# Kernel optimization log

Hardware: AMD Instinct MI355X
Metric: run time of the kernel (lower is better)

Reference implementation:

```python
import jax, jax.numpy as jnp
import numpy as np

N = 100000      # nodes
E = 1600000     # edges (before self-loops)
IN = 128        # in_dim
HID = 128       # hidden_dim
H = 4           # heads
D = HID // H    # head_dim = 32
L = 3           # n_layers
G = 128         # graphs in batch
NEG_SLOPE = 0.2 # PyG GATConv default leaky_relu slope
BN_EPS = 1e-5


def setup_inputs() -> dict:
    key = jax.random.key(0)
    ks = jax.random.split(key, 16)
    x = jax.random.normal(ks[0], (N, IN), dtype=jnp.float32)
    edge_index = jax.random.randint(ks[1], (2, E), 0, N, dtype=jnp.int64)
    batch = jnp.sort(jax.random.randint(ks[2], (N,), 0, G, dtype=jnp.int64))
    # stacked per-layer GATConv params (in_dim == hidden_dim so all layers stack)
    W = jax.random.normal(ks[3], (L, HID, HID), dtype=jnp.float32) * (1.0 / np.sqrt(HID))
    att_src = jax.random.normal(ks[4], (L, H, D), dtype=jnp.float32) * 0.1
    att_dst = jax.random.normal(ks[5], (L, H, D), dtype=jnp.float32) * 0.1
    bias = jax.random.normal(ks[6], (L, HID), dtype=jnp.float32) * 0.01
    # BatchNorm1d (eval mode: running stats)
    gamma = 1.0 + 0.1 * jax.random.normal(ks[7], (L, HID), dtype=jnp.float32)
    beta = 0.01 * jax.random.normal(ks[8], (L, HID), dtype=jnp.float32)
    bn_mean = jnp.zeros((L, HID), dtype=jnp.float32)
    bn_var = jnp.ones((L, HID), dtype=jnp.float32)
    # MLP head: Linear(HID, HID//2) -> ReLU -> Linear(HID//2, 1)
    Wh1 = jax.random.normal(ks[9], (HID, HID // 2), dtype=jnp.float32) * (1.0 / np.sqrt(HID))
    bh1 = jnp.zeros((HID // 2,), dtype=jnp.float32)
    Wh2 = jax.random.normal(ks[10], (HID // 2, 1), dtype=jnp.float32) * (1.0 / np.sqrt(HID // 2))
    bh2 = jnp.zeros((1,), dtype=jnp.float32)
    return {"x": x, "edge_index": edge_index, "batch": batch, "W": W,
            "att_src": att_src, "att_dst": att_dst, "bias": bias,
            "gamma": gamma, "beta": beta, "bn_mean": bn_mean, "bn_var": bn_var,
            "Wh1": Wh1, "bh1": bh1, "Wh2": Wh2, "bh2": bh2}


def _gat_conv(x, src, dst, W_l, asrc, adst, b):
    # x: [N, F_in]; src/dst: [E+N] (self-loops included); returns [N, H*D]
    h = (x @ W_l).reshape(N, H, D)                      # [N,H,D]
    a_s = jnp.einsum('nhd,hd->nh', h, asrc)             # [N,H]
    a_d = jnp.einsum('nhd,hd->nh', h, adst)
    e = jax.nn.leaky_relu(a_s[src] + a_d[dst], NEG_SLOPE)  # [Etot,H]
    # segment softmax over incoming edges per destination node
    e_max = jax.ops.segment_max(e, dst, num_segments=N)    # [N,H]
    p = jnp.exp(e - e_max[dst])
    denom = jax.ops.segment_sum(p, dst, num_segments=N)    # [N,H]
    alpha = p / (denom[dst] + 1e-16)                        # [Etot,H]
    msg = h[src] * alpha[:, :, None]                        # [Etot,H,D]
    out = jax.ops.segment_sum(msg, dst, num_segments=N)     # [N,H,D]
    return out.reshape(N, H * D) + b


def reference(x, edge_index, batch, W, att_src, att_dst, bias,
              gamma, beta, bn_mean, bn_var, Wh1, bh1, Wh2, bh2):
    # add self-loops once (PyG GATConv default add_self_loops=True)
    loop = jnp.arange(N, dtype=edge_index.dtype)
    src = jnp.concatenate([edge_index[0], loop])
    dst = jnp.concatenate([edge_index[1], loop])
    for l in range(L):
        x = _gat_conv(x, src, dst, W[l], att_src[l], att_dst[l], bias[l])
        x = jnp.maximum(x, 0.0)
        # BatchNorm1d, eval mode (dropout is identity in eval)
        x = (x - bn_mean[l]) * (gamma[l] / jnp.sqrt(bn_var[l] + BN_EPS)) + beta[l]
    # global mean pool over graphs
    sums = jax.ops.segment_sum(x, batch, num_segments=G)            # [G,HID]
    cnts = jax.ops.segment_sum(jnp.ones((N,), x.dtype), batch, num_segments=G)
    pooled = sums / jnp.maximum(cnts, 1.0)[:, None]
    hdn = jnp.maximum(pooled @ Wh1 + bh1, 0.0)
    return (hdn @ Wh2 + bh2).squeeze(-1)                            # [G]
```

## Files before the change

### kernel.cpp

```cpp
#include <hip/hip_runtime.h>
#include <hip/hip_fp16.h>


typedef __bf16 bf16x8 __attribute__((ext_vector_type(8)));
typedef float  f32x4  __attribute__((ext_vector_type(4)));
typedef unsigned int u32x4 __attribute__((ext_vector_type(4)));

#define WLSZ 36864
#define MAXBKT 800
#define BCAP   4096

__device__ __forceinline__ int foff(int l, int d, int n, int k) {
    int ct = n >> 4, li = n & 15;
    int ks = k >> 5, bq = (k >> 3) & 3, j = k & 7;
    return l * WLSZ + (((ks * 18) + d * 9 + ct) * 64 + (bq << 4) + li) * 8 + j;
}

__global__ __launch_bounds__(256)
void k_front(const int* __restrict__ ei, unsigned int* __restrict__ bkt,
             int* __restrict__ bcnt, float* __restrict__ gsum,
             int* __restrict__ gcnt, const int* __restrict__ batch,
             const float* __restrict__ gamma, const float* __restrict__ beta,
             const float* __restrict__ mean, const float* __restrict__ var,
             float* __restrict__ bn_mul, float* __restrict__ bn_add,
             const float* __restrict__ W, const float* __restrict__ asrc,
             const float* __restrict__ adst, __bf16* __restrict__ WF,
             int Ne, int Nn, int nbkt, int Gg, int nBB) {
    __shared__ int lcnt[MAXBKT];
    __shared__ int lbase[MAXBKT];
    int bb = blockIdx.x;
    int tid = threadIdx.x;

    if (bb < nBB) {
        int gid = bb * 256 + tid;
        if (gid < Gg * 128) gsum[gid] = 0.f;
        for (int i = tid; i < nbkt; i += 256) lcnt[i] = 0;
        __syncthreads();
        int chunk0 = bb * 2048;
        int nnz = Ne + Nn;
        for (int i = 0; i < 8; ++i) {
            int e = chunk0 + i * 256 + tid;
            if (e < nnz) {
                int d = (e < Ne) ? ei[Ne + e] : (e - Ne);
                atomicAdd(&lcnt[d >> 7], 1);
            }
        }
        __syncthreads();
        for (int b = tid; b < nbkt; b += 256) {
            int c = lcnt[b];
            lbase[b] = (c > 0) ? atomicAdd(&bcnt[b], c) : 0;
            lcnt[b] = 0;
        }
        __syncthreads();
        for (int i = 0; i < 8; ++i) {
            int e = chunk0 + i * 256 + tid;
            if (e < nnz) {
                int s, d;
                if (e < Ne) { s = ei[e]; d = ei[Ne + e]; }
                else        { s = e - Ne; d = e - Ne; }
                int b = d >> 7;
                int r = atomicAdd(&lcnt[b], 1);
                bkt[(long)b * BCAP + lbase[b] + r] = ((unsigned)s << 7) | (unsigned)(d & 127);
            }
        }
    } else if (bb < nBB + 192) {
        int gid = (bb - nBB) * 256 + tid;
        if (gid < 384) {
            float sc = gamma[gid] / sqrtf(var[gid] + 1e-5f);
            bn_mul[gid] = sc;
            bn_add[gid] = beta[gid] - mean[gid] * sc;
        }
        if (gid < 3 * 128 * 128) {
            int l = gid >> 14;
            int k = (gid >> 7) & 127;
            int n = gid & 127;
            float f = W[gid];
            __bf16 h = (__bf16)f;
            WF[foff(l, 0, n, k)] = h;
            WF[foff(l, 1, n, k)] = (__bf16)(f - (float)h);
        }
        if (gid < 3 * 128 * 8) {
            int l = gid >> 10;
            int r = gid & 1023;
            int k = r >> 3;
            int j = r & 7;
            int hh = j & 3;
            const float* av = (j < 4 ? asrc : adst) + l * 128 + hh * 32;
            const float* wp = W + l * 16384 + k * 128 + hh * 32;
            float sum = 0.f;
#pragma unroll
            for (int d = 0; d < 32; ++d) sum = fmaf(wp[d], av[d], sum);
            __bf16 h = (__bf16)sum;
            WF[foff(l, 0, 128 + j, k)] = h;
            WF[foff(l, 1, 128 + j, k)] = (__bf16)(sum - (float)h);
        }
        if (gid < 3 * 128 * 8) {
            int l = gid >> 10;
            int r = gid & 1023;
            int k = r >> 3;
            int j = r & 7;
            WF[foff(l, 0, 136 + j, k)] = (__bf16)0.f;
            WF[foff(l, 1, 136 + j, k)] = (__bf16)0.f;
        }
    } else {
        int g = tid;
        if (g < Gg) {
            int lo = 0, hi = Nn;
            while (lo < hi) { int mid = (lo + hi) >> 1; if (batch[mid] < g) lo = mid + 1; else hi = mid; }
            int lo2 = lo, hi2 = Nn;
            while (lo2 < hi2) { int mid = (lo2 + hi2) >> 1; if (batch[mid] < g + 1) lo2 = mid + 1; else hi2 = mid; }
            gcnt[g] = lo2 - lo;
        }
    }
}

__global__ __launch_bounds__(256)
void k_bscatter2(const unsigned int* __restrict__ bkt, const int* __restrict__ bcnt,
                 int* __restrict__ rowstart, int* __restrict__ rowdeg,
                 int* __restrict__ colv, int Nn) {
    __shared__ int h[128], sc0[128], sc1[128];
    int b = blockIdx.x;
    int tid = threadIdx.x;
    if (tid < 128) h[tid] = 0;
    __syncthreads();
    int cnt = bcnt[b];
    const unsigned int* bp = bkt + (long)b * BCAP;
    for (int i = tid; i < cnt; i += 256) atomicAdd(&h[bp[i] & 127], 1);
    __syncthreads();
    int cntN = (tid < 128) ? h[tid] : 0;
    if (tid < 128) sc0[tid] = cntN;
    __syncthreads();
    int* src = sc0; int* dst = sc1;
    for (int off = 1; off < 128; off <<= 1) {
        if (tid < 128) {
            int x = src[tid];
            if (tid >= off) x += src[tid - off];
            dst[tid] = x;
        }
        __syncthreads();
        int* tw = src; src = dst; dst = tw;
    }
    int node = b * 128 + tid;
    if (tid < 128) {
        int st = b * BCAP + (src[tid] - cntN);
        h[tid] = st;
        if (node < Nn) { rowstart[node] = st; rowdeg[node] = cntN; }
    }
    __syncthreads();
    for (int i = tid; i < cnt; i += 256) {
        unsigned int e = bp[i];
        int pos = atomicAdd(&h[e & 127], 1);
        colv[pos] = (int)(e >> 7);
    }
}

__global__ __launch_bounds__(256, 4)
void k_gemm_mfma(const float* __restrict__ X, const __bf16* __restrict__ WF,
                 __half* __restrict__ Hout,
                 float* __restrict__ as_, float* __restrict__ ad_, int Nn) {
    int t = threadIdx.x;
    int w = t >> 6;
    int lane = t & 63;
    int li = lane & 15;
    int b  = lane >> 4;
    long row = (long)blockIdx.x * 64 + w * 16 + li;
    long rA = (row > Nn - 1) ? (Nn - 1) : row;

    f32x4 acc[9];
#pragma unroll
    for (int ct = 0; ct < 9; ++ct) acc[ct] = (f32x4){0.f, 0.f, 0.f, 0.f};

#pragma unroll
    for (int ks = 0; ks < 4; ++ks) {
        int k0 = ks * 32 + 8 * b;
        const float* xp = X + rA * 128 + k0;
        float4 f0 = *(const float4*)xp;
        float4 f1 = *(const float4*)(xp + 4);
        float af[8] = {f0.x, f0.y, f0.z, f0.w, f1.x, f1.y, f1.z, f1.w};
        bf16x8 ahi, alo;
#pragma unroll
        for (int j = 0; j < 8; ++j) {
            __bf16 h = (__bf16)af[j];
            ahi[j] = h;
            alo[j] = (__bf16)(af[j] - (float)h);
        }
        const __bf16* wk = WF + (ks * 18) * 512 + lane * 8;
#pragma unroll
        for (int ct = 0; ct < 9; ++ct) {
            bf16x8 bhi = *(const bf16x8*)(wk + ct * 512);
            bf16x8 blo = *(const bf16x8*)(wk + (9 + ct) * 512);
            acc[ct] = __builtin_amdgcn_mfma_f32_16x16x32_bf16(bhi, ahi, acc[ct], 0, 0, 0);
            acc[ct] = __builtin_amdgcn_mfma_f32_16x16x32_bf16(bhi, alo, acc[ct], 0, 0, 0);
            acc[ct] = __builtin_amdgcn_mfma_f32_16x16x32_bf16(blo, ahi, acc[ct], 0, 0, 0);
        }
    }

    if (row < Nn) {
        __half* op = Hout + row * 128 + 4 * b;
#pragma unroll
        for (int ct = 0; ct < 8; ++ct) {
            union { __half2 h2[2]; uint2 u; } pk;
            pk.h2[0] = __floats2half2_rn(acc[ct][0], acc[ct][1]);
            pk.h2[1] = __floats2half2_rn(acc[ct][2], acc[ct][3]);
            *(uint2*)(op + ct * 16) = pk.u;
        }
        if (b == 0)
            *(float4*)(as_ + 4 * row) = make_float4(acc[8][0], acc[8][1],
                                                    acc[8][2], acc[8][3]);
        else if (b == 1)
            *(float4*)(ad_ + 4 * row) = make_float4(acc[8][0], acc[8][1],
                                                    acc[8][2], acc[8][3]);
    }
}

#define LEAKY(x) ((x) > 0.f ? (x) : 0.2f * (x))

template <bool POOL>
__global__ __launch_bounds__(256)
void k_aggregate(const __half* __restrict__ Hb, const float* __restrict__ as_,
                 const float* __restrict__ ad_, const int* __restrict__ rowstart,
                 const int* __restrict__ rowdeg,
                 const int* __restrict__ col, const float* __restrict__ bias,
                 const float* __restrict__ bn_mul, const float* __restrict__ bn_add,
                 float* __restrict__ Xout, const int* __restrict__ batch,
                 float* __restrict__ gsum, int Nn) {
    __shared__ int2 s_pk[4][64][4];
    __shared__ float s_out[POOL ? 4 : 1][POOL ? 128 : 1];
    __shared__ int s_g[POOL ? 4 : 1];
    int w = threadIdx.x >> 6;
    int n = (blockIdx.x << 2) + w;
    int lane = threadIdx.x & 63;
    bool active = (n < Nn);
    if (!POOL && !active) return;
    if (POOL && lane == 0) s_g[w] = active ? batch[n] : -1;

    if (active) {
        int start = rowstart[n];
        int deg = rowdeg[n];

        if (deg <= 64) {
            int hh = lane & 3;
            int slot = lane >> 2;
            float adn = ad_[4 * n + hh];
            float esc[4]; int scl[4];
#pragma unroll
            for (int c = 0; c < 4; ++c) {
                int eidx = (c << 4) + slot;
                float e = -1e30f; int s = 0;
                if (eidx < deg) {
                    s = col[start + eidx];
                    e = LEAKY(as_[4 * s + hh] + adn);
                }
                esc[c] = e; scl[c] = s;
            }
            float m = fmaxf(fmaxf(esc[0], esc[1]), fmaxf(esc[2], esc[3]));
#pragma unroll
            for (int msk = 4; msk < 64; msk <<= 1) m = fmaxf(m, __shfl_xor(m, msk, 64));
            float p[4];
            float den = 0.f;
#pragma unroll
            for (int c = 0; c < 4; ++c) { p[c] = __expf(esc[c] - m); den += p[c]; }
#pragma unroll
            for (int msk = 4; msk < 64; msk <<= 1) den += __shfl_xor(den, msk, 64);
            float inv = 1.f / (den + 1e-16f);
#pragma unroll
            for (int c = 0; c < 4; ++c) {
                int2 pk;
                pk.x = scl[c] << 8;
                pk.y = __float_as_int(p[c] * inv);
                s_pk[w][(c << 4) + slot][hh] = pk;
            }

            int quarter = lane >> 4;
            int li = lane & 15;
            int hB = li >> 2;
            int cByte = li << 4;
            const char* hb8 = (const char*)Hb;
            float acc[8];
#pragma unroll
            for (int i = 0; i < 8; ++i) acc[i] = 0.f;

            int nit = (deg + 7) >> 3;
            int2 pk0 = s_pk[w][quarter][hB];
            int2 pk1 = s_pk[w][quarter + 4][hB];
            float a0 = __int_as_float(pk0.y);
            float a1 = __int_as_float(pk1.y);
            u32x4 r0 = *(const u32x4*)(hb8 + pk0.x + cByte);
            u32x4 r1 = *(const u32x4*)(hb8 + pk1.x + cByte);
            for (int it = 1; it < nit; ++it) {
                int e0 = (it << 3) + quarter;
                int2 q0 = s_pk[w][e0][hB];
                int2 q1 = s_pk[w][e0 + 4][hB];
                u32x4 t0 = *(const u32x4*)(hb8 + q0.x + cByte);
                u32x4 t1 = *(const u32x4*)(hb8 + q1.x + cByte);
                const __half* h0 = (const __half*)&r0;
                const __half* h1 = (const __half*)&r1;
#pragma unroll
                for (int q = 0; q < 8; ++q) {
                    acc[q] = fmaf(__half2float(h0[q]), a0, acc[q]);
                    acc[q] = fmaf(__half2float(h1[q]), a1, acc[q]);
                }
                r0 = t0; r1 = t1;
                a0 = __int_as_float(q0.y);
                a1 = __int_as_float(q1.y);
            }
            {
                const __half* h0 = (const __half*)&r0;
                const __half* h1 = (const __half*)&r1;
#pragma unroll
                for (int q = 0; q < 8; ++q) {
                    acc[q] = fmaf(__half2float(h0[q]), a0, acc[q]);
                    acc[q] = fmaf(__half2float(h1[q]), a1, acc[q]);
                }
            }
#pragma unroll
            for (int i = 0; i < 8; ++i) {
                float v = acc[i];
                v += __shfl_xor(v, 16, 64);
                v += __shfl_xor(v, 32, 64);
                acc[i] = v;
            }
            if (lane < 16) {
                int c0 = li << 3;
                float4 bz0 = *(const float4*)(bias + c0);
                float4 bz1 = *(const float4*)(bias + c0 + 4);
                float4 m0 = *(const float4*)(bn_mul + c0);
                float4 m1 = *(const float4*)(bn_mul + c0 + 4);
                float4 a0v = *(const float4*)(bn_add + c0);
                float4 a1v = *(const float4*)(bn_add + c0 + 4);
                float4 o0, o1;
                o0.x = fmaf(fmaxf(acc[0] + bz0.x, 0.f), m0.x, a0v.x);
                o0.y = fmaf(fmaxf(acc[1] + bz0.y, 0.f), m0.y, a0v.y);
                o0.z = fmaf(fmaxf(acc[2] + bz0.z, 0.f), m0.z, a0v.z);
                o0.w = fmaf(fmaxf(acc[3] + bz0.w, 0.f), m0.w, a0v.w);
                o1.x = fmaf(fmaxf(acc[4] + bz1.x, 0.f), m1.x, a1v.x);
                o1.y = fmaf(fmaxf(acc[5] + bz1.y, 0.f), m1.y, a1v.y);
                o1.z = fmaf(fmaxf(acc[6] + bz1.z, 0.f), m1.z, a1v.z);
                o1.w = fmaf(fmaxf(acc[7] + bz1.w, 0.f), m1.w, a1v.w);
                if (!POOL) {
                    *(float4*)(Xout + (long)n * 128 + c0)     = o0;
                    *(float4*)(Xout + (long)n * 128 + c0 + 4) = o1;
                } else {
                    *(float4*)(&s_out[w][c0])     = o0;
                    *(float4*)(&s_out[w][c0 + 4]) = o1;
                }
            }
        } else {
            int end = start + deg;
            int hh = lane & 3;
            float adn = ad_[n * 4 + hh];
            float m = -1e30f;
            for (int base = start; base < end; base += 16) {
                int idx = base + (lane >> 2);
                float sc = -1e30f;
                if (idx < end) {
                    int s = col[idx];
                    float e = as_[s * 4 + hh] + adn;
                    sc = LEAKY(e);
                }
                m = fmaxf(m, sc);
            }
            for (int msk = 4; msk < 64; msk <<= 1) m = fmaxf(m, __shfl_xor(m, msk, 64));
            float den = 0.f;
            for (int base = start; base < end; base += 16) {
                int idx = base + (lane >> 2);
                if (idx < end) {
                    int s = col[idx];
                    float e = as_[s * 4 + hh] + adn;
                    e = LEAKY(e);
                    den += __expf(e - m);
                }
            }
            for (int msk = 4; msk < 64; msk <<= 1) den += __shfl_xor(den, msk, 64);
            int hB = lane >> 4;
            float mB   = __shfl(m, hB, 64);
            float invB = 1.f / (__shfl(den, hB, 64) + 1e-16f);
            float adB  = ad_[n * 4 + hB];
            int c0 = lane << 1;
            float acc0 = 0.f, acc1 = 0.f;
            for (int i = start; i < end; ++i) {
                int s = col[i];
                float e = as_[s * 4 + hB] + adB;
                e = LEAKY(e);
                float alpha = __expf(e - mB) * invB;
                float2 hv = __half22float2(*(const __half2*)(Hb + (long)s * 128 + c0));
                acc0 = fmaf(hv.x, alpha, acc0);
                acc1 = fmaf(hv.y, alpha, acc1);
            }
            float v0 = acc0 + bias[c0], v1 = acc1 + bias[c0 + 1];
            v0 = fmaxf(v0, 0.f); v1 = fmaxf(v1, 0.f);
            v0 = fmaf(v0, bn_mul[c0], bn_add[c0]);
            v1 = fmaf(v1, bn_mul[c0 + 1], bn_add[c0 + 1]);
            if (!POOL) {
                *(float2*)(Xout + (long)n * 128 + c0) = make_float2(v0, v1);
            } else {
                s_out[w][c0]     = v0;
                s_out[w][c0 + 1] = v1;
            }
        }
    } else if (POOL) {
        if (lane < 16) {
            int c0 = (lane & 15) << 3;
#pragma unroll
            for (int i = 0; i < 8; ++i) s_out[w][c0 + i] = 0.f;
        }
    }

    if (POOL) {
        __syncthreads();
        int tid = threadIdx.x;
        if (tid < 128) {
            int g0 = s_g[0], g1 = s_g[1], g2 = s_g[2], g3 = s_g[3];
            float v0 = s_out[0][tid], v1 = s_out[1][tid];
            float v2 = s_out[2][tid], v3 = s_out[3][tid];
            if (g0 == g1 && g1 == g2 && g2 == g3) {
                if (g0 >= 0) atomicAdd(&gsum[g0 * 128 + tid], v0 + v1 + v2 + v3);
            } else {
                if (g0 >= 0) atomicAdd(&gsum[g0 * 128 + tid], v0);
                if (g1 >= 0) atomicAdd(&gsum[g1 * 128 + tid], v1);
                if (g2 >= 0) atomicAdd(&gsum[g2 * 128 + tid], v2);
                if (g3 >= 0) atomicAdd(&gsum[g3 * 128 + tid], v3);
            }
        }
    }
}

__global__ __launch_bounds__(64)
void k_head(const float* __restrict__ gsum, const int* __restrict__ gcnt,
            const float* __restrict__ Wh1, const float* __restrict__ bh1,
            const float* __restrict__ Wh2, const float* __restrict__ bh2,
            float* __restrict__ outp) {
    __shared__ float pooled[128];
    int g = blockIdx.x;
    int j = threadIdx.x;
    int cnt = gcnt[g];
    float inv = 1.f / (float)(cnt > 1 ? cnt : 1);
    pooled[j]      = gsum[g * 128 + j] * inv;
    pooled[j + 64] = gsum[g * 128 + 64 + j] * inv;
    __syncthreads();
    float acc = bh1[j];
    for (int k = 0; k < 128; ++k) acc = fmaf(pooled[k], Wh1[k * 64 + j], acc);
    acc = fmaxf(acc, 0.f);
    float prod = acc * Wh2[j];
    for (int msk = 1; msk < 64; msk <<= 1) prod += __shfl_xor(prod, msk, 64);
    if (j == 0) outp[g] = prod + bh2[0];
}

extern "C" void kernel_launch(void* const* d_in, const int* in_sizes, int n_in,
                              void* d_out, int out_size, void* d_ws, size_t ws_size,
                              hipStream_t stream) {
    const float* x       = (const float*)d_in[0];
    const int*   ei      = (const int*)d_in[1];
    const int*   batch   = (const int*)d_in[2];
    const float* W       = (const float*)d_in[3];
    const float* att_src = (const float*)d_in[4];
    const float* att_dst = (const float*)d_in[5];
    const float* bias    = (const float*)d_in[6];
    const float* gamma   = (const float*)d_in[7];
    const float* beta    = (const float*)d_in[8];
    const float* bn_mean = (const float*)d_in[9];
    const float* bn_var  = (const float*)d_in[10];
    const float* Wh1     = (const float*)d_in[11];
    const float* bh1     = (const float*)d_in[12];
    const float* Wh2     = (const float*)d_in[13];
    const float* bh2     = (const float*)d_in[14];
    float* out = (float*)d_out;

    const int Nn = in_sizes[0] / 128;
    const int Ne = in_sizes[1] / 2;
    const int Gg = out_size;
    const int nnz = Ne + Nn;
    const int nbkt = (Nn + 127) / 128;
    const int nBB = (nnz + 2047) / 2048;

    char* ws = (char*)d_ws;
    size_t off = 0;
    auto alloc = [&](size_t bytes) -> char* {
        char* p = ws + off;
        off = (off + bytes + 255) & ~(size_t)255;
        return p;
    };
    float*        bufA     = (float*)alloc((size_t)Nn * 128 * 4);
    __half*       bufH     = (__half*)alloc((size_t)Nn * 128 * 2);
    float*        as_      = (float*)alloc((size_t)Nn * 4 * 4);
    float*        ad_      = (float*)alloc((size_t)Nn * 4 * 4);
    int*          rowstart = (int*)alloc((size_t)Nn * 4);
    int*          rowdeg   = (int*)alloc((size_t)Nn * 4);
    int*          col      = (int*)alloc((size_t)nbkt * BCAP * 4);
    float*        bn_mul   = (float*)alloc(384 * 4);
    float*        bn_add   = (float*)alloc(384 * 4);
    float*        gsum     = (float*)alloc((size_t)Gg * 128 * 4);
    int*          gcnt     = (int*)alloc((size_t)Gg * 4);
    __bf16*       WtF      = (__bf16*)alloc((size_t)3 * WLSZ * 2);
    unsigned int* bkt      = (unsigned int*)alloc((size_t)nbkt * BCAP * 4);
    int*          bcnt     = (int*)alloc((size_t)nbkt * 4);

    hipMemsetAsync(bcnt, 0, (size_t)nbkt * 4, stream);
    k_front<<<nBB + 193, 256, 0, stream>>>(ei, bkt, bcnt, gsum, gcnt, batch,
                                           gamma, beta, bn_mean, bn_var,
                                           bn_mul, bn_add, W, att_src, att_dst,
                                           WtF, Ne, Nn, nbkt, Gg, nBB);
    k_bscatter2<<<nbkt, 256, 0, stream>>>(bkt, bcnt, rowstart, rowdeg, col, Nn);

    const float* cur = x;
    for (int l = 0; l < 3; ++l) {
        k_gemm_mfma<<<(Nn + 63) / 64, 256, 0, stream>>>(cur, WtF + l * WLSZ,
                                                        bufH, as_, ad_, Nn);
        if (l < 2)
            k_aggregate<false><<<(Nn + 3) / 4, 256, 0, stream>>>(
                bufH, as_, ad_, rowstart, rowdeg, col, bias + l * 128,
                bn_mul + l * 128, bn_add + l * 128, bufA, batch, gsum, Nn);
        else
            k_aggregate<true><<<(Nn + 3) / 4, 256, 0, stream>>>(
                bufH, as_, ad_, rowstart, rowdeg, col, bias + l * 128,
                bn_mul + l * 128, bn_add + l * 128, bufA, batch, gsum, Nn);
        cur = bufA;
    }

    k_head<<<Gg, 64, 0, stream>>>(gsum, gcnt, Wh1, bh1, Wh2, bh2, out);
}
```

Baseline: 504.2 us.

## Process two nodes per wavefront in GAT aggregation when both degrees are small

Restructures the aggregation kernel so each 64-lane wavefront handles two destination nodes, one per 32-lane half, whenever both have degree at most 32, which is the common case with an average degree near 17. The goal is to cut the idle lanes and per-node overhead of the earlier one-node-per-wave scheme, where most softmax slots and gather lanes did nothing. Pairs that include a higher-degree node fall back to processing the two nodes one after another with the old full-wave and big-degree paths. The cost is more shuffle and branch logic, scalar rather than vectorised output stores, and a slowdown when either node in a pair exceeds 32 edges.

Measured after the change: 506.7 us. No clear change (+0.5%).

```diff
diff --git a/kernel.cpp b/kernel.cpp
--- a/kernel.cpp
+++ b/kernel.cpp
@@ -215,6 +215,153 @@
 
 #define LEAKY(x) ((x) > 0.f ? (x) : 0.2f * (x))
 
+__device__ __forceinline__ void agg_full(
+    const __half* __restrict__ Hb, const float* __restrict__ as_,
+    const float* __restrict__ ad_, const int* __restrict__ col,
+    const float* __restrict__ bias, const float* __restrict__ bn_mul,
+    const float* __restrict__ bn_add, int2 (*spk)[4],
+    int n, int start, int deg, int lane, float* orow) {
+    int hh = lane & 3;
+    int slot = lane >> 2;
+    float adn = ad_[4 * n + hh];
+    float esc[4]; int scl[4];
+#pragma unroll
+    for (int c = 0; c < 4; ++c) {
+        int eidx = (c << 4) + slot;
+        float e = -1e30f; int s = 0;
+        if (eidx < deg) {
+            s = col[start + eidx];
+            e = LEAKY(as_[4 * s + hh] + adn);
+        }
+        esc[c] = e; scl[c] = s;
+    }
+    float m = fmaxf(fmaxf(esc[0], esc[1]), fmaxf(esc[2], esc[3]));
+#pragma unroll
+    for (int msk = 4; msk < 64; msk <<= 1) m = fmaxf(m, __shfl_xor(m, msk, 64));
+    float p[4];
+    float den = 0.f;
+#pragma unroll
+    for (int c = 0; c < 4; ++c) { p[c] = __expf(esc[c] - m); den += p[c]; }
+#pragma unroll
+    for (int msk = 4; msk < 64; msk <<= 1) den += __shfl_xor(den, msk, 64);
+    float inv = 1.f / (den + 1e-16f);
+#pragma unroll
+    for (int c = 0; c < 4; ++c) {
+        int2 pk;
+        pk.x = scl[c] << 8;
+        pk.y = __float_as_int(p[c] * inv);
+        spk[(c << 4) + slot][hh] = pk;
+    }
+
+    int quarter = lane >> 4;
+    int li = lane & 15;
+    int hB = li >> 2;
+    int cByte = li << 4;
+    const char* hb8 = (const char*)Hb;
+    float acc[8];
+#pragma unroll
+    for (int i = 0; i < 8; ++i) acc[i] = 0.f;
+
+    int nit = (deg + 7) >> 3;
+    int2 pk0 = spk[quarter][hB];
+    int2 pk1 = spk[quarter + 4][hB];
+    float a0 = __int_as_float(pk0.y);
+    float a1 = __int_as_float(pk1.y);
+    u32x4 r0 = *(const u32x4*)(hb8 + pk0.x + cByte);
+    u32x4 r1 = *(const u32x4*)(hb8 + pk1.x + cByte);
+    for (int it = 1; it < nit; ++it) {
+        int e0 = (it << 3) + quarter;
+        int2 q0 = spk[e0][hB];
+        int2 q1 = spk[e0 + 4][hB];
+        u32x4 t0 = *(const u32x4*)(hb8 + q0.x + cByte);
+        u32x4 t1 = *(const u32x4*)(hb8 + q1.x + cByte);
+        const __half* h0 = (const __half*)&r0;
+        const __half* h1 = (const __half*)&r1;
+#pragma unroll
+        for (int q = 0; q < 8; ++q) {
+            acc[q] = fmaf(__half2float(h0[q]), a0, acc[q]);
+            acc[q] = fmaf(__half2float(h1[q]), a1, acc[q]);
+        }
+        r0 = t0; r1 = t1;
+        a0 = __int_as_float(q0.y);
+        a1 = __int_as_float(q1.y);
+    }
+    {
+        const __half* h0 = (const __half*)&r0;
+        const __half* h1 = (const __half*)&r1;
+#pragma unroll
+        for (int q = 0; q < 8; ++q) {
+            acc[q] = fmaf(__half2float(h0[q]), a0, acc[q]);
+            acc[q] = fmaf(__half2float(h1[q]), a1, acc[q]);
+        }
+    }
+#pragma unroll
+    for (int i = 0; i < 8; ++i) {
+        float v = acc[i];
+        v += __shfl_xor(v, 16, 64);
+        v += __shfl_xor(v, 32, 64);
+        acc[i] = v;
+    }
+    if (lane < 16) {
+        int c0 = li << 3;
+#pragma unroll
+        for (int i = 0; i < 8; ++i) {
+            float v = fmaxf(acc[i] + bias[c0 + i], 0.f);
+            orow[c0 + i] = fmaf(v, bn_mul[c0 + i], bn_add[c0 + i]);
+        }
+    }
+}
+
+__device__ __forceinline__ void agg_big(
+    const __half* __restrict__ Hb, const float* __restrict__ as_,
+    const float* __restrict__ ad_, const int* __restrict__ col,
+    const float* __restrict__ bias, const float* __restrict__ bn_mul,
+    const float* __restrict__ bn_add,
+    int n, int start, int deg, int lane, float* orow) {
+    int end = start + deg;
+    int hh = lane & 3;
+    float adn = ad_[n * 4 + hh];
+    float m = -1e30f;
+    for (int base = start; base < end; base += 16) {
+        int idx = base + (lane >> 2);
+        float sc = -1e30f;
+        if (idx < end) {
+            int s = col[idx];
+            sc = LEAKY(as_[s * 4 + hh] + adn);
+        }
+        m = fmaxf(m, sc);
+    }
+    for (int msk = 4; msk < 64; msk <<= 1) m = fmaxf(m, __shfl_xor(m, msk, 64));
+    float den = 0.f;
+    for (int base = start; base < end; base += 16) {
+        int idx = base + (lane >> 2);
+        if (idx < end) {
+            int s = col[idx];
+            float e = LEAKY(as_[s * 4 + hh] + adn);
+            den += __expf(e - m);
+        }
+    }
+    for (int msk = 4; msk < 64; msk <<= 1) den += __shfl_xor(den, msk, 64);
+    int hB = lane >> 4;
+    float mB   = __shfl(m, hB, 64);
+    float invB = 1.f / (__shfl(den, hB, 64) + 1e-16f);
+    float adB  = ad_[n * 4 + hB];
+    int c0 = lane << 1;
+    float acc0 = 0.f, acc1 = 0.f;
+    for (int i = start; i < end; ++i) {
+        int s = col[i];
+        float e = LEAKY(as_[s * 4 + hB] + adB);
+        float alpha = __expf(e - mB) * invB;
+        float2 hv = __half22float2(*(const __half2*)(Hb + (long)s * 128 + c0));
+        acc0 = fmaf(hv.x, alpha, acc0);
+        acc1 = fmaf(hv.y, alpha, acc1);
+    }
+    float v0 = fmaxf(acc0 + bias[c0], 0.f);
+    float v1 = fmaxf(acc1 + bias[c0 + 1], 0.f);
+    orow[c0]     = fmaf(v0, bn_mul[c0], bn_add[c0]);
+    orow[c0 + 1] = fmaf(v1, bn_mul[c0 + 1], bn_add[c0 + 1]);
+}
+
 template <bool POOL>
 __global__ __launch_bounds__(256)
 void k_aggregate(const __half* __restrict__ Hb, const float* __restrict__ as_,
@@ -225,184 +372,136 @@
                  float* __restrict__ Xout, const int* __restrict__ batch,
                  float* __restrict__ gsum, int Nn) {
     __shared__ int2 s_pk[4][64][4];
-    __shared__ float s_out[POOL ? 4 : 1][POOL ? 128 : 1];
-    __shared__ int s_g[POOL ? 4 : 1];
+    __shared__ float s_out[POOL ? 8 : 1][POOL ? 128 : 1];
+    __shared__ int s_g[POOL ? 8 : 1];
     int w = threadIdx.x >> 6;
-    int n = (blockIdx.x << 2) + w;
     int lane = threadIdx.x & 63;
-    bool active = (n < Nn);
-    if (!POOL && !active) return;
-    if (POOL && lane == 0) s_g[w] = active ? batch[n] : -1;
-
-    if (active) {
-        int start = rowstart[n];
-        int deg = rowdeg[n];
-
-        if (deg <= 64) {
-            int hh = lane & 3;
-            int slot = lane >> 2;
-            float adn = ad_[4 * n + hh];
-            float esc[4]; int scl[4];
-#pragma unroll
-            for (int c = 0; c < 4; ++c) {
-                int eidx = (c << 4) + slot;
-                float e = -1e30f; int s = 0;
-                if (eidx < deg) {
-                    s = col[start + eidx];
-                    e = LEAKY(as_[4 * s + hh] + adn);
+    int half = lane >> 5;
+    int hl = lane & 31;
+    int nbase = (blockIdx.x << 3) + (w << 1);
+    int n = nbase + half;
+    bool active = n < Nn;
+    if (!POOL && nbase >= Nn) return;
+    if (POOL && hl == 0) s_g[(w << 1) + half] = active ? batch[n] : -1;
+
+    int start = active ? rowstart[n] : 0;
+    int deg   = active ? rowdeg[n]   : 0;
+    int degO  = __shfl_xor(deg, 32, 64);
+    int degmax = deg > degO ? deg : degO;
+
+    if (degmax <= 32) {
+        int hh = hl & 3;
+        int slot = hl >> 2;
+        float adn = active ? ad_[4 * n + hh] : 0.f;
+        float esc[4]; int scl[4];
+#pragma unroll
+        for (int c = 0; c < 4; ++c) {
+            int eidx = (c << 3) + slot;
+            float e = -1e30f; int s = 0;
+            if (eidx < deg) {
+                s = col[start + eidx];
+                e = LEAKY(as_[4 * s + hh] + adn);
+            }
+            esc[c] = e; scl[c] = s;
+        }
+        float m = fmaxf(fmaxf(esc[0], esc[1]), fmaxf(esc[2], esc[3]));
+#pragma unroll
+        for (int msk = 4; msk < 32; msk <<= 1) m = fmaxf(m, __shfl_xor(m, msk, 64));
+        float p[4];
+        float den = 0.f;
+#pragma unroll
+        for (int c = 0; c < 4; ++c) { p[c] = __expf(esc[c] - m); den += p[c]; }
+#pragma unroll
+        for (int msk = 4; msk < 32; msk <<= 1) den += __shfl_xor(den, msk, 64);
+        float inv = 1.f / (den + 1e-16f);
+        int hbase = half << 5;
+#pragma unroll
+        for (int c = 0; c < 4; ++c) {
+            int2 pk;
+            pk.x = scl[c] << 8;
+            pk.y = __float_as_int(p[c] * inv);
+            s_pk[w][hbase + (c << 3) + slot][hh] = pk;
+        }
+
+        int q = (hl >> 4) & 1;
+        int li = hl & 15;
+        int hB = li >> 2;
+        int cByte = li << 4;
+        const char* hb8 = (const char*)Hb;
+        float acc[8];
+#pragma unroll
+        for (int i = 0; i < 8; ++i) acc[i] = 0.f;
+
+        int nit = (degmax + 3) >> 2;
+        int2 pk0 = s_pk[w][hbase + q][hB];
+        int2 pk1 = s_pk[w][hbase + q + 2][hB];
+        float a0 = __int_as_float(pk0.y);
+        float a1 = __int_as_float(pk1.y);
+        u32x4 r0 = *(const u32x4*)(hb8 + pk0.x + cByte);
+        u32x4 r1 = *(const u32x4*)(hb8 + pk1.x + cByte);
+        for (int it = 1; it < nit; ++it) {
+            int e0 = (it << 2) + q;
+            int2 q0 = s_pk[w][hbase + e0][hB];
+            int2 q1 = s_pk[w][hbase + e0 + 2][hB];
+            u32x4 t0 = *(const u32x4*)(hb8 + q0.x + cByte);
+            u32x4 t1 = *(const u32x4*)(hb8 + q1.x + cByte);
+            const __half* h0 = (const __half*)&r0;
+            const __half* h1 = (const __half*)&r1;
+#pragma unroll
+            for (int qq = 0; qq < 8; ++qq) {
+                acc[qq] = fmaf(__half2float(h0[qq]), a0, acc[qq]);
+                acc[qq] = fmaf(__half2float(h1[qq]), a1, acc[qq]);
+            }
+            r0 = t0; r1 = t1;
+            a0 = __int_as_float(q0.y);
+            a1 = __int_as_float(q1.y);
+        }
+        {
+            const __half* h0 = (const __half*)&r0;
+            const __half* h1 = (const __half*)&r1;
+#pragma unroll
+            for (int qq = 0; qq < 8; ++qq) {
+                acc[qq] = fmaf(__half2float(h0[qq]), a0, acc[qq]);
+                acc[qq] = fmaf(__half2float(h1[qq]), a1, acc[qq]);
+            }
+        }
+#pragma unroll
+        for (int i = 0; i < 8; ++i) acc[i] += __shfl_xor(acc[i], 16, 64);
+
+        if (hl < 16) {
+            int c0 = li << 3;
+            if (active) {
+#pragma unroll
+                for (int i = 0; i < 8; ++i) {
+                    float v = fmaxf(acc[i] + bias[c0 + i], 0.f);
+                    v = fmaf(v, bn_mul[c0 + i], bn_add[c0 + i]);
+                    if (!POOL) Xout[(long)n * 128 + c0 + i] = v;
+                    else       s_out[(w << 1) + half][c0 + i] = v;
                 }
-                esc[c] = e; scl[c] = s;
-            }
-            float m = fmaxf(fmaxf(esc[0], esc[1]), fmaxf(esc[2], esc[3]));
-#pragma unroll
-            for (int msk = 4; msk < 64; msk <<= 1) m = fmaxf(m, __shfl_xor(m, msk, 64));
-            float p[4];
-            float den = 0.f;
-#pragma unroll
-            for (int c = 0; c < 4; ++c) { p[c] = __expf(esc[c] - m); den += p[c]; }
-#pragma unroll
-            for (int msk = 4; msk < 64; msk <<= 1) den += __shfl_xor(den, msk, 64);
-            float inv = 1.f / (den + 1e-16f);
-#pragma unroll
-            for (int c = 0; c < 4; ++c) {
-                int2 pk;
-                pk.x = scl[c] << 8;
-                pk.y = __float_as_int(p[c] * inv);
-                s_pk[w][(c << 4) + slot][hh] = pk;
-            }
-
-            int quarter = lane >> 4;
-            int li = lane & 15;
-            int hB = li >> 2;
-            int cByte = li << 4;
-            const char* hb8 = (const char*)Hb;
-            float acc[8];
-#pragma unroll
-            for (int i = 0; i < 8; ++i) acc[i] = 0.f;
-
-            int nit = (deg + 7) >> 3;
-            int2 pk0 = s_pk[w][quarter][hB];
-            int2 pk1 = s_pk[w][quarter + 4][hB];
-            float a0 = __int_as_float(pk0.y);
-            float a1 = __int_as_float(pk1.y);
-            u32x4 r0 = *(const u32x4*)(hb8 + pk0.x + cByte);
-            u32x4 r1 = *(const u32x4*)(hb8 + pk1.x + cByte);
-            for (int it = 1; it < nit; ++it) {
-                int e0 = (it << 3) + quarter;
-                int2 q0 = s_pk[w][e0][hB];
-                int2 q1 = s_pk[w][e0 + 4][hB];
-                u32x4 t0 = *(const u32x4*)(hb8 + q0.x + cByte);
-                u32x4 t1 = *(const u32x4*)(hb8 + q1.x + cByte);
-                const __half* h0 = (const __half*)&r0;
-                const __half* h1 = (const __half*)&r1;
-#pragma unroll
-                for (int q = 0; q < 8; ++q) {
-                    acc[q] = fmaf(__half2float(h0[q]), a0, acc[q]);
-                    acc[q] = fmaf(__half2float(h1[q]), a1, acc[q]);
-                }
-                r0 = t0; r1 = t1;
-                a0 = __int_as_float(q0.y);
-                a1 = __int_as_float(q1.y);
-            }
-            {
-                const __half* h0 = (const __half*)&r0;
-                const __half* h1 = (const __half*)&r1;
-#pragma unroll
-                for (int q = 0; q < 8; ++q) {
-                    acc[q] = fmaf(__half2float(h0[q]), a0, acc[q]);
-                    acc[q] = fmaf(__half2float(h1[q]), a1, acc[q]);
-                }
-            }
-#pragma unroll
-            for (int i = 0; i < 8; ++i) {
-                float v = acc[i];
-                v += __shfl_xor(v, 16, 64);
-                v += __shfl_xor(v, 32, 64);
-                acc[i] = v;
-            }
-            if (lane < 16) {
-                int c0 = li << 3;
-                float4 bz0 = *(const float4*)(bias + c0);
-                float4 bz1 = *(const float4*)(bias + c0 + 4);
-                float4 m0 = *(const float4*)(bn_mul + c0);
-                float4 m1 = *(const float4*)(bn_mul + c0 + 4);
-                float4 a0v = *(const float4*)(bn_add + c0);
-                float4 a1v = *(const float4*)(bn_add + c0 + 4);
-                float4 o0, o1;
-                o0.x = fmaf(fmaxf(acc[0] + bz0.x, 0.f), m0.x, a0v.x);
-                o0.y = fmaf(fmaxf(acc[1] + bz0.y, 0.f), m0.y, a0v.y);
-                o0.z = fmaf(fmaxf(acc[2] + bz0.z, 0.f), m0.z, a0v.z);
-                o0.w = fmaf(fmaxf(acc[3] + bz0.w, 0.f), m0.w, a0v.w);
-                o1.x = fmaf(fmaxf(acc[4] + bz1.x, 0.f), m1.x, a1v.x);
-                o1.y = fmaf(fmaxf(acc[5] + bz1.y, 0.f), m1.y, a1v.y);
-                o1.z = fmaf(fmaxf(acc[6] + bz1.z, 0.f), m1.z, a1v.z);
-                o1.w = fmaf(fmaxf(acc[7] + bz1.w, 0.f), m1.w, a1v.w);
-                if (!POOL) {
-                    *(float4*)(Xout + (long)n * 128 + c0)     = o0;
-                    *(float4*)(Xout + (long)n * 128 + c0 + 4) = o1;
-                } else {
-                    *(float4*)(&s_out[w][c0])     = o0;
-                    *(float4*)(&s_out[w][c0 + 4]) = o1;
-                }
-            }
-        } else {
-            int end = start + deg;
-            int hh = lane & 3;
-            float adn = ad_[n * 4 + hh];
-            float m = -1e30f;
-            for (int base = start; base < end; base += 16) {
-                int idx = base + (lane >> 2);
-                float sc = -1e30f;
-                if (idx < end) {
-                    int s = col[idx];
-                    float e = as_[s * 4 + hh] + adn;
-                    sc = LEAKY(e);
-                }
-                m = fmaxf(m, sc);
-            }
-            for (int msk = 4; msk < 64; msk <<= 1) m = fmaxf(m, __shfl_xor(m, msk, 64));
-            float den = 0.f;
-            for (int base = start; base < end; base += 16) {
-                int idx = base + (lane >> 2);
-                if (idx < end) {
-                    int s = col[idx];
-                    float e = as_[s * 4 + hh] + adn;
-                    e = LEAKY(e);
-                    den += __expf(e - m);
-                }
-            }
-            for (int msk = 4; msk < 64; msk <<= 1) den += __shfl_xor(den, msk, 64);
-            int hB = lane >> 4;
-            float mB   = __shfl(m, hB, 64);
-            float invB = 1.f / (__shfl(den, hB, 64) + 1e-16f);
-            float adB  = ad_[n * 4 + hB];
-            int c0 = lane << 1;
-            float acc0 = 0.f, acc1 = 0.f;
-            for (int i = start; i < end; ++i) {
-                int s = col[i];
-                float e = as_[s * 4 + hB] + adB;
-                e = LEAKY(e);
-                float alpha = __expf(e - mB) * invB;
-                float2 hv = __half22float2(*(const __half2*)(Hb + (long)s * 128 + c0));
-                acc0 = fmaf(hv.x, alpha, acc0);
-                acc1 = fmaf(hv.y, alpha, acc1);
-            }
-            float v0 = acc0 + bias[c0], v1 = acc1 + bias[c0 + 1];
-            v0 = fmaxf(v0, 0.f); v1 = fmaxf(v1, 0.f);
-            v0 = fmaf(v0, bn_mul[c0], bn_add[c0]);
-            v1 = fmaf(v1, bn_mul[c0 + 1], bn_add[c0 + 1]);
-            if (!POOL) {
-                *(float2*)(Xout + (long)n * 128 + c0) = make_float2(v0, v1);
-            } else {
-                s_out[w][c0]     = v0;
-                s_out[w][c0 + 1] = v1;
-            }
-        }
-    } else if (POOL) {
-        if (lane < 16) {
-            int c0 = (lane & 15) << 3;
-#pragma unroll
-            for (int i = 0; i < 8; ++i) s_out[w][c0 + i] = 0.f;
+            } else if (POOL) {
+#pragma unroll
+                for (int i = 0; i < 8; ++i) s_out[(w << 1) + half][c0 + i] = 0.f;
+            }
+        }
+    } else {
+        for (int h2 = 0; h2 < 2; ++h2) {
+            int nn = nbase + h2;
+            int st2 = __shfl(start, h2 << 5, 64);
+            int dg2 = __shfl(deg, h2 << 5, 64);
+            bool act2 = nn < Nn;
+            float* orow;
+            if (POOL) orow = &s_out[(w << 1) + h2][0];
+            else      orow = Xout + (long)nn * 128;
+            if (act2) {
+                if (dg2 <= 64)
+                    agg_full(Hb, as_, ad_, col, bias, bn_mul, bn_add,
+                             s_pk[w], nn, st2, dg2, lane, orow);
+                else
+                    agg_big(Hb, as_, ad_, col, bias, bn_mul, bn_add,
+                            nn, st2, dg2, lane, orow);
+            } else if (POOL) {
+                for (int i = lane; i < 128; i += 64) orow[i] = 0.f;
+            }
         }
     }
 
@@ -410,16 +509,21 @@
         __syncthreads();
         int tid = threadIdx.x;
         if (tid < 128) {
-            int g0 = s_g[0], g1 = s_g[1], g2 = s_g[2], g3 = s_g[3];
-            float v0 = s_out[0][tid], v1 = s_out[1][tid];
-            float v2 = s_out[2][tid], v3 = s_out[3][tid];
-            if (g0 == g1 && g1 == g2 && g2 == g3) {
-                if (g0 >= 0) atomicAdd(&gsum[g0 * 128 + tid], v0 + v1 + v2 + v3);
+            int g0 = s_g[0];
+            bool same = true;
+#pragma unroll
+            for (int k = 1; k < 8; ++k) same = same && (s_g[k] == g0);
+            if (same) {
+                if (g0 >= 0) {
+                    float s8 = 0.f;
+#pragma unroll
+                    for (int k = 0; k < 8; ++k) s8 += s_out[k][tid];
+                    atomicAdd(&gsum[g0 * 128 + tid], s8);
+                }
             } else {
-                if (g0 >= 0) atomicAdd(&gsum[g0 * 128 + tid], v0);
-                if (g1 >= 0) atomicAdd(&gsum[g1 * 128 + tid], v1);
-                if (g2 >= 0) atomicAdd(&gsum[g2 * 128 + tid], v2);
-                if (g3 >= 0) atomicAdd(&gsum[g3 * 128 + tid], v3);
+#pragma unroll
+                for (int k = 0; k < 8; ++k)
+                    if (s_g[k] >= 0) atomicAdd(&gsum[s_g[k] * 128 + tid], s_out[k][tid]);
             }
         }
     }
@@ -507,11 +611,11 @@
         k_gemm_mfma<<<(Nn + 63) / 64, 256, 0, stream>>>(cur, WtF + l * WLSZ,
                                                         bufH, as_, ad_, Nn);
         if (l < 2)
-            k_aggregate<false><<<(Nn + 3) / 4, 256, 0, stream>>>(
+            k_aggregate<false><<<(Nn + 7) / 8, 256, 0, stream>>>(
                 bufH, as_, ad_, rowstart, rowdeg, col, bias + l * 128,
                 bn_mul + l * 128, bn_add + l * 128, bufA, batch, gsum, Nn);
         else
-            k_aggregate<true><<<(Nn + 3) / 4, 256, 0, stream>>>(
+            k_aggregate<true><<<(Nn + 7) / 8, 256, 0, stream>>>(
                 bufH, as_, ad_, rowstart, rowdeg, col, bias + l * 128,
                 bn_mul + l * 128, bn_add + l * 128, bufA, batch, gsum, Nn);
         cur = bufA;
```
